# Kernel optimization log

Measured on AMD Instinct MI355X. Metric: run time of the kernel, lower is better.

The kernel has to match this reference:

```python
import jax, jax.numpy as jnp
import numpy as np

B, T, D, F, E, TOPK = 4, 2048, 1024, 2752, 8, 2


def setup_inputs() -> dict:
    key = jax.random.key(0)
    k1, k2, k3, k4 = jax.random.split(key, 4)
    x = jax.random.normal(k1, (B, T, D), dtype=jnp.float32)
    # Expert params, torch Linear(bias=False) stored as [in, out] for x @ W
    W13 = jax.random.normal(k2, (E, D, 2 * F), dtype=jnp.float32) * 0.02  # gate+up packed
    W2 = jax.random.normal(k3, (E, F, D), dtype=jnp.float32) * 0.02       # down proj
    Wr = jax.random.normal(k4, (D, E), dtype=jnp.float32) * 0.02          # router
    return {"x": x, "W13": W13, "W2": W2, "Wr": Wr}


def reference(x, W13, W2, Wr):
    b, t, d = x.shape
    xf = x.reshape(-1, d)                       # [N, D]
    n = xf.shape[0]
    logits = xf @ Wr                            # [N, E]
    probs = jax.nn.softmax(logits, axis=-1)
    top_probs, top_idx = jax.lax.top_k(probs, TOPK)  # [N, K]
    top_probs = top_probs / top_probs.sum(axis=-1, keepdims=True)
    # combine weights: cw[n, e] = sum_k top_probs[n, k] * (top_idx[n, k] == e)
    cw = jnp.zeros((n, E), dtype=xf.dtype).at[jnp.arange(n)[:, None], top_idx].add(top_probs)
    out = jnp.zeros_like(xf)
    for e in range(E):  # small fixed expert loop; tokens with cw==0 contribute nothing
        x13 = xf @ W13[e]                       # [N, 2F]
        x1, x3 = jnp.split(x13, 2, axis=-1)
        h = jax.nn.silu(x1) * x3                # SwiGLU
        out = out + cw[:, e:e + 1] * (h @ W2[e])
    return out.reshape(b, t, d)
```

## Files before the change

kernel.cpp:

```cpp
#include <hip/hip_runtime.h>
#include <stdint.h>

#define NTOK 8192
#define DDIM 1024
#define FDIM 2752
#define NEXP 8
#define DF2  5504
#define NSLOT 16384
#define NT1 16
#define NT2 43

typedef __attribute__((ext_vector_type(8))) short bf16x8;
typedef __attribute__((ext_vector_type(4))) float f32x4;
typedef __attribute__((ext_vector_type(4))) unsigned short u16x4;
typedef __attribute__((ext_vector_type(8))) unsigned short u16x8;

constexpr size_t XB_OFF   = 0;
constexpr size_t XB_SZ    = (size_t)NTOK * DDIM * 2;
constexpr size_t W13T_OFF = XB_OFF + XB_SZ;
constexpr size_t W13T_SZ  = (size_t)NEXP * DF2 * DDIM * 2;
constexpr size_t W2T_OFF  = W13T_OFF + W13T_SZ;
constexpr size_t W2T_SZ   = (size_t)NEXP * DDIM * FDIM * 2;
constexpr size_t H_OFF    = W2T_OFF + W2T_SZ;
constexpr size_t H_SZ     = (size_t)NSLOT * FDIM * 2;
constexpr size_t ST_OFF   = H_OFF + H_SZ;
constexpr size_t SW_OFF   = ST_OFF + (size_t)NSLOT * 4;
constexpr size_t TTI_OFF  = SW_OFF + (size_t)NSLOT * 4;
constexpr size_t TTW_OFF  = TTI_OFF + (size_t)NTOK * 8;
constexpr size_t META_OFF = TTW_OFF + (size_t)NTOK * 8;
constexpr size_t TS_OFF   = META_OFF + 256;

__device__ __forceinline__ unsigned short f2bf(float f) {
  unsigned u = __float_as_uint(f);
  u += 0x7FFFu + ((u >> 16) & 1u);
  return (unsigned short)(u >> 16);
}

__device__ __forceinline__ void gl_lds16(const void* g, void* l) {
  __builtin_amdgcn_global_load_lds(
      (const __attribute__((address_space(1))) unsigned int*)g,
      (__attribute__((address_space(3))) unsigned int*)l, 16, 0, 0);
}

#define BARF()  do { asm volatile("" ::: "memory"); __builtin_amdgcn_s_barrier(); asm volatile("" ::: "memory"); } while (0)
#define LGKM0   asm volatile("s_waitcnt lgkmcnt(0)" ::: "memory")
#define GATE6   asm volatile("s_waitcnt vmcnt(6)" ::: "memory")
#define GATE4   asm volatile("s_waitcnt vmcnt(4)" ::: "memory")
#define VM0     asm volatile("s_waitcnt vmcnt(0)" ::: "memory")
#define PRIO1   __builtin_amdgcn_s_setprio(1)
#define PRIO0   __builtin_amdgcn_s_setprio(0)
#define MFMA16(aa, bb, cc) cc = __builtin_amdgcn_mfma_f32_16x16x32_bf16(aa, bb, cc, 0, 0, 0)

#define STG(dstbase, parr, koff)                        \
  do {                                                  \
    gl_lds16(parr[0] + (koff), (dstbase) + sdst);       \
    gl_lds16(parr[1] + (koff), (dstbase) + sdst + 512); \
  } while (0)

__global__ void cvt_x_k(const float* __restrict__ x, unsigned short* __restrict__ xb) {
  int i = blockIdx.x * 256 + threadIdx.x;
  float4 v = ((const float4*)x)[i];
  u16x4 o;
  o[0] = f2bf(v.x); o[1] = f2bf(v.y); o[2] = f2bf(v.z); o[3] = f2bf(v.w);
  ((u16x4*)xb)[i] = o;
}

__global__ void tcvt_k(const float* __restrict__ src, unsigned short* __restrict__ dst,
                       int R, int C) {
  __shared__ unsigned short tile[64][65];
  long base = (long)blockIdx.z * R * C;
  src += base; dst += base;
  int r0 = blockIdx.y * 64, c0 = blockIdx.x * 64;
  int t = threadIdx.x;
  int rr = t >> 4, cc = (t & 15) * 4;
  for (int i = 0; i < 4; ++i) {
    float4 v = *(const float4*)&src[(long)(r0 + rr + i * 16) * C + c0 + cc];
    tile[rr + i * 16][cc + 0] = f2bf(v.x);
    tile[rr + i * 16][cc + 1] = f2bf(v.y);
    tile[rr + i * 16][cc + 2] = f2bf(v.z);
    tile[rr + i * 16][cc + 3] = f2bf(v.w);
  }
  __syncthreads();
  int dr = t >> 2, sg = (t & 3) * 16;
  u16x8 o0, o1;
  for (int i = 0; i < 8; ++i) { o0[i] = tile[sg + i][dr]; o1[i] = tile[sg + 8 + i][dr]; }
  unsigned short* dp = &dst[(long)(c0 + dr) * R + r0 + sg];
  *(u16x8*)dp = o0;
  *(u16x8*)(dp + 8) = o1;
}

__global__ void router_k(const float* __restrict__ x, const float* __restrict__ Wr,
                         int* __restrict__ meta, int2* __restrict__ tt_i,
                         float2* __restrict__ tt_w) {
  int lane = threadIdx.x & 63;
  int tok = blockIdx.x * 4 + (threadIdx.x >> 6);
  float acc[8];
#pragma unroll
  for (int e = 0; e < 8; ++e) acc[e] = 0.f;
  const float4* xr = (const float4*)(x + (long)tok * DDIM);
#pragma unroll
  for (int it = 0; it < 4; ++it) {
    float4 v = xr[it * 64 + lane];
    int d = (it * 64 + lane) * 4;
    float xv[4] = {v.x, v.y, v.z, v.w};
#pragma unroll
    for (int j = 0; j < 4; ++j) {
      const float4* wr = (const float4*)(Wr + (long)(d + j) * NEXP);
      float4 wa = wr[0], wb = wr[1];
      acc[0] += xv[j] * wa.x; acc[1] += xv[j] * wa.y;
      acc[2] += xv[j] * wa.z; acc[3] += xv[j] * wa.w;
      acc[4] += xv[j] * wb.x; acc[5] += xv[j] * wb.y;
      acc[6] += xv[j] * wb.z; acc[7] += xv[j] * wb.w;
    }
  }
#pragma unroll
  for (int e = 0; e < 8; ++e)
    for (int off = 32; off; off >>= 1) acc[e] += __shfl_xor(acc[e], off, 64);
  if (lane == 0) {
    float m = acc[0];
    for (int e = 1; e < 8; ++e) m = fmaxf(m, acc[e]);
    float p[8];
    for (int e = 0; e < 8; ++e) p[e] = __expf(acc[e] - m);
    int e0 = 0;
    for (int e = 1; e < 8; ++e) if (p[e] > p[e0]) e0 = e;
    int e1 = -1;
    for (int e = 0; e < 8; ++e) { if (e == e0) continue; if (e1 < 0 || p[e] > p[e1]) e1 = e; }
    float s = p[e0] + p[e1];
    atomicAdd(&meta[e0], 1);
    atomicAdd(&meta[e1], 1);
    tt_i[tok] = make_int2(e0, e1);
    tt_w[tok] = make_float2(p[e0] / s, p[e1] / s);
  }
}

__global__ void offsets_k(int* meta) {
  int run = 0;
  for (int e = 0; e < NEXP; ++e) { meta[16 + e] = run; run += meta[e]; }
}

__global__ void scatter_k(const int2* __restrict__ tt_i, const float2* __restrict__ tt_w,
                          int* __restrict__ meta, int* __restrict__ slot_tok,
                          float* __restrict__ slot_w, int2* __restrict__ tok_slot) {
  int n = blockIdx.x * 256 + threadIdx.x;
  int2 ei = tt_i[n];
  float2 wv = tt_w[n];
  int p0 = atomicAdd(&meta[8 + ei.x], 1);
  int s0 = meta[16 + ei.x] + p0;
  slot_tok[s0] = n; slot_w[s0] = wv.x;
  int p1 = atomicAdd(&meta[8 + ei.y], 1);
  int s1 = meta[16 + ei.y] + p1;
  slot_tok[s1] = n; slot_w[s1] = wv.y;
  tok_slot[n] = make_int2(s0, s1);
}

__global__ __launch_bounds__(512, 2) void gemm1_k(
    const unsigned short* __restrict__ xb, const unsigned short* __restrict__ w13t,
    const int* __restrict__ meta, const int* __restrict__ slot_tok,
    unsigned short* __restrict__ h) {
  int e = blockIdx.z;
  int n_e = meta[e];
  int m0 = blockIdx.y * 256;
  if (m0 >= n_e) return;
  int base = meta[16 + e];
  int c0 = blockIdx.x * 128;
  const unsigned short* wB = w13t + (long)e * DF2 * DDIM;

  __shared__ unsigned short Ab[2][2][8192];
  __shared__ unsigned short Bb[2][2][8192];

  int t = threadIdx.x;
  int lane = t & 63, w = t >> 6;
  int wm = w >> 2, wn = w & 3;
  int fr = lane & 15;

  int rj = w * 16 + (lane >> 3);
  int kc = ((lane & 7) ^ ((lane >> 4) & 2)) * 8;
  int sdst = w * 1024 + lane * 8;

  const unsigned short* pA[2][2];
  const unsigned short* pB[2][2];
#pragma unroll
  for (int hh = 0; hh < 2; ++hh)
#pragma unroll
    for (int j = 0; j < 2; ++j) {
      int tr = hh * 128 + rj + j * 8;
      int tok = slot_tok[base + min(m0 + tr, n_e - 1)];
      pA[hh][j] = xb + (long)tok * DDIM + kc;
      int wr = (tr < 128) ? min(c0 + tr, FDIM - 1) : FDIM + min(c0 + tr - 128, FDIM - 1);
      pB[hh][j] = wB + (long)wr * DDIM + kc;
    }

  int qp = ((lane >> 4) ^ ((lane >> 2) & 1) * 2) * 8;
  int abase = fr * 64 + qp;
  int bbase = wn * 2048 + fr * 64 + qp;

  f32x4 acc[8][4];
#pragma unroll
  for (int mi = 0; mi < 8; ++mi)
#pragma unroll
    for (int n = 0; n < 4; ++n) acc[mi][n] = (f32x4){0.f, 0.f, 0.f, 0.f};
  bf16x8 a[8], b0, b1;

  STG(&Ab[0][0][0], pA[0], 0);
  STG(&Ab[0][1][0], pA[1], 0);
  STG(&Bb[0][0][0], pB[0], 0);
  STG(&Bb[0][1][0], pB[1], 0);
  STG(&Bb[1][0][0], pB[0], (1 < NT1) ? 64 : 0);
  GATE4;
  BARF();

#pragma unroll 1
  for (int U = 0; U < NT1; ++U) {
    int cur = U & 1, nxt = cur ^ 1;
    const unsigned short* Ac = &Ab[cur][wm][0];
    const unsigned short* B0c = &Bb[cur][0][0];
    const unsigned short* B1c = &Bb[cur][1][0];
    int k1 = ((U + 1) < NT1) ? (U + 1) * 64 : 0;
    int k2 = ((U + 2) < NT1) ? (U + 2) * 64 : 0;
#pragma unroll
    for (int mi = 0; mi < 8; ++mi) a[mi] = *(const bf16x8*)&Ac[mi * 1024 + abase];
    b0 = *(const bf16x8*)&B0c[bbase];
    b1 = *(const bf16x8*)&B0c[1024 + bbase];
    STG(&Ab[nxt][0][0], pA[0], k1);
    BARF(); LGKM0;
    PRIO1;
#pragma unroll
    for (int mi = 0; mi < 8; ++mi) { MFMA16(a[mi], b0, acc[mi][0]); MFMA16(a[mi], b1, acc[mi][1]); }
    PRIO0;
    GATE4;
    BARF();
    b0 = *(const bf16x8*)&B1c[bbase];
    b1 = *(const bf16x8*)&B1c[1024 + bbase];
    STG(&Ab[nxt][1][0], pA[1], k1);
    BARF(); LGKM0;
    PRIO1;
#pragma unroll
    for (int mi = 0; mi < 8; ++mi) { MFMA16(a[mi], b0, acc[mi][2]); MFMA16(a[mi], b1, acc[mi][3]); }
    PRIO0;
    BARF();
#pragma unroll
    for (int mi = 0; mi < 8; ++mi) a[mi] = *(const bf16x8*)&Ac[mi * 1024 + 32 + abase];
    b0 = *(const bf16x8*)&B0c[32 + bbase];
    b1 = *(const bf16x8*)&B0c[1024 + 32 + bbase];
    STG(&Bb[nxt][1][0], pB[1], k1);
    BARF(); LGKM0;
    PRIO1;
#pragma unroll
    for (int mi = 0; mi < 8; ++mi) { MFMA16(a[mi], b0, acc[mi][0]); MFMA16(a[mi], b1, acc[mi][1]); }
    PRIO0;
    GATE6;
    BARF();
    b0 = *(const bf16x8*)&B1c[32 + bbase];
    b1 = *(const bf16x8*)&B1c[1024 + 32 + bbase];
    STG(&Bb[cur][0][0], pB[0], k2);
    BARF(); LGKM0;
    PRIO1;
#pragma unroll
    for (int mi = 0; mi < 8; ++mi) { MFMA16(a[mi], b0, acc[mi][2]); MFMA16(a[mi], b1, acc[mi][3]); }
    PRIO0;
    GATE4;
    BARF();
  }
  VM0;

  int quad = lane >> 4;
#pragma unroll
  for (int mi = 0; mi < 8; ++mi)
#pragma unroll
    for (int r = 0; r < 4; ++r) {
      int m = m0 + wm * 128 + mi * 16 + quad * 4 + r;
      if (m < n_e) {
        unsigned short* hp = &h[(long)(base + m) * FDIM];
#pragma unroll
        for (int n = 0; n < 2; ++n) {
          int col = c0 + wn * 32 + n * 16 + fr;
          if (col < FDIM) {
            float g = acc[mi][n][r], u = acc[mi][n + 2][r];
            hp[col] = f2bf((g / (1.f + __expf(-g))) * u);
          }
        }
      }
    }
}

__global__ __launch_bounds__(512, 2) void gemm2_k(
    const unsigned short* __restrict__ hb, const unsigned short* __restrict__ w2t,
    const int* __restrict__ meta, const float* __restrict__ slot_w,
    float* __restrict__ y) {
  int e = blockIdx.z;
  int n_e = meta[e];
  int m0 = blockIdx.y * 256;
  if (m0 >= n_e) return;
  int base = meta[16 + e];
  int c0 = blockIdx.x * 256;
  const unsigned short* wB = w2t + (long)e * DDIM * FDIM;

  __shared__ unsigned short Ab[2][2][8192];
  __shared__ unsigned short Bb[2][2][8192];

  int t = threadIdx.x;
  int lane = t & 63, w = t >> 6;
  int wm = w >> 2, wn = w & 3;
  int fr = lane & 15;

  int rj = w * 16 + (lane >> 3);
  int kc = ((lane & 7) ^ ((lane >> 4) & 2)) * 8;
  int sdst = w * 1024 + lane * 8;

  const unsigned short* pA[2][2];
  const unsigned short* pB[2][2];
#pragma unroll
  for (int hh = 0; hh < 2; ++hh)
#pragma unroll
    for (int j = 0; j < 2; ++j) {
      int tr = hh * 128 + rj + j * 8;
      int srow = base + min(m0 + tr, n_e - 1);
      pA[hh][j] = hb + (long)srow * FDIM + kc;
      pB[hh][j] = wB + (long)(c0 + tr) * FDIM + kc;
    }

  int qp = ((lane >> 4) ^ ((lane >> 2) & 1) * 2) * 8;
  int abase = fr * 64 + qp;
  int bbase = wn * 2048 + fr * 64 + qp;

  f32x4 acc[8][4];
#pragma unroll
  for (int mi = 0; mi < 8; ++mi)
#pragma unroll
    for (int n = 0; n < 4; ++n) acc[mi][n] = (f32x4){0.f, 0.f, 0.f, 0.f};
  bf16x8 a[8], b0, b1;

  STG(&Ab[0][0][0], pA[0], 0);
  STG(&Ab[0][1][0], pA[1], 0);
  STG(&Bb[0][0][0], pB[0], 0);
  STG(&Bb[0][1][0], pB[1], 0);
  STG(&Bb[1][0][0], pB[0], (1 < NT2) ? 64 : 0);
  GATE4;
  BARF();

#pragma unroll 1
  for (int U = 0; U < NT2; ++U) {
    int cur = U & 1, nxt = cur ^ 1;
    const unsigned short* Ac = &Ab[cur][wm][0];
    const unsigned short* B0c = &Bb[cur][0][0];
    const unsigned short* B1c = &Bb[cur][1][0];
    int k1 = ((U + 1) < NT2) ? (U + 1) * 64 : 0;
    int k2 = ((U + 2) < NT2) ? (U + 2) * 64 : 0;
#pragma unroll
    for (int mi = 0; mi < 8; ++mi) a[mi] = *(const bf16x8*)&Ac[mi * 1024 + abase];
    b0 = *(const bf16x8*)&B0c[bbase];
    b1 = *(const bf16x8*)&B0c[1024 + bbase];
    STG(&Ab[nxt][0][0], pA[0], k1);
    BARF(); LGKM0;
    PRIO1;
#pragma unroll
    for (int mi = 0; mi < 8; ++mi) { MFMA16(a[mi], b0, acc[mi][0]); MFMA16(a[mi], b1, acc[mi][1]); }
    PRIO0;
    GATE4;
    BARF();
    b0 = *(const bf16x8*)&B1c[bbase];
    b1 = *(const bf16x8*)&B1c[1024 + bbase];
    STG(&Ab[nxt][1][0], pA[1], k1);
    BARF(); LGKM0;
    PRIO1;
#pragma unroll
    for (int mi = 0; mi < 8; ++mi) { MFMA16(a[mi], b0, acc[mi][2]); MFMA16(a[mi], b1, acc[mi][3]); }
    PRIO0;
    BARF();
#pragma unroll
    for (int mi = 0; mi < 8; ++mi) a[mi] = *(const bf16x8*)&Ac[mi * 1024 + 32 + abase];
    b0 = *(const bf16x8*)&B0c[32 + bbase];
    b1 = *(const bf16x8*)&B0c[1024 + 32 + bbase];
    STG(&Bb[nxt][1][0], pB[1], k1);
    BARF(); LGKM0;
    PRIO1;
#pragma unroll
    for (int mi = 0; mi < 8; ++mi) { MFMA16(a[mi], b0, acc[mi][0]); MFMA16(a[mi], b1, acc[mi][1]); }
    PRIO0;
    GATE6;
    BARF();
    b0 = *(const bf16x8*)&B1c[32 + bbase];
    b1 = *(const bf16x8*)&B1c[1024 + 32 + bbase];
    STG(&Bb[cur][0][0], pB[0], k2);
    BARF(); LGKM0;
    PRIO1;
#pragma unroll
    for (int mi = 0; mi < 8; ++mi) { MFMA16(a[mi], b0, acc[mi][2]); MFMA16(a[mi], b1, acc[mi][3]); }
    PRIO0;
    GATE4;
    BARF();
  }
  VM0;

  int quad = lane >> 4;
#pragma unroll
  for (int mi = 0; mi < 8; ++mi)
#pragma unroll
    for (int r = 0; r < 4; ++r) {
      int m = m0 + wm * 128 + mi * 16 + quad * 4 + r;
      if (m < n_e) {
        float wgt = slot_w[base + m];
        float* yp = y + (long)(base + m) * DDIM;
#pragma unroll
        for (int n = 0; n < 4; ++n) {
          int col = c0 + (n >> 1) * 128 + wn * 32 + (n & 1) * 16 + fr;
          yp[col] = wgt * acc[mi][n][r];
        }
      }
    }
}

__global__ void combine_k(const float* __restrict__ y, const int2* __restrict__ tok_slot,
                          float* __restrict__ out) {
  int tok = blockIdx.x * 4 + (threadIdx.x >> 6);
  int lane = threadIdx.x & 63;
  int2 s = tok_slot[tok];
  const float4* y0 = (const float4*)(y + (long)s.x * DDIM);
  const float4* y1 = (const float4*)(y + (long)s.y * DDIM);
  float4* o = (float4*)(out + (long)tok * DDIM);
#pragma unroll
  for (int i = 0; i < 4; ++i) {
    float4 u = y0[i * 64 + lane], v = y1[i * 64 + lane];
    o[i * 64 + lane] = make_float4(u.x + v.x, u.y + v.y, u.z + v.z, u.w + v.w);
  }
}

extern "C" void kernel_launch(void* const* d_in, const int* in_sizes, int n_in,
                              void* d_out, int out_size, void* d_ws, size_t ws_size,
                              hipStream_t stream) {
  const float* x   = (const float*)d_in[0];
  const float* W13 = (const float*)d_in[1];
  const float* W2  = (const float*)d_in[2];
  const float* Wr  = (const float*)d_in[3];
  float* out = (float*)d_out;
  char* ws = (char*)d_ws;

  unsigned short* xb   = (unsigned short*)(ws + XB_OFF);
  unsigned short* w13t = (unsigned short*)(ws + W13T_OFF);
  unsigned short* w2t  = (unsigned short*)(ws + W2T_OFF);
  unsigned short* hbuf = (unsigned short*)(ws + H_OFF);
  int*    slot_tok = (int*)(ws + ST_OFF);
  float*  slot_w   = (float*)(ws + SW_OFF);
  int2*   tt_i     = (int2*)(ws + TTI_OFF);
  float2* tt_w     = (float2*)(ws + TTW_OFF);
  int*    meta     = (int*)(ws + META_OFF);
  int2*   tok_slot = (int2*)(ws + TS_OFF);
  float*  ybuf     = (float*)(ws + W13T_OFF);

  hipMemsetAsync(meta, 0, 128, stream);

  cvt_x_k<<<NTOK * DDIM / 4 / 256, 256, 0, stream>>>(x, xb);
  tcvt_k<<<dim3(DF2 / 64, DDIM / 64, NEXP), 256, 0, stream>>>(W13, w13t, DDIM, DF2);
  tcvt_k<<<dim3(DDIM / 64, FDIM / 64, NEXP), 256, 0, stream>>>(W2, w2t, FDIM, DDIM);
  router_k<<<NTOK / 4, 256, 0, stream>>>(x, Wr, meta, tt_i, tt_w);
  offsets_k<<<1, 1, 0, stream>>>(meta);
  scatter_k<<<NTOK / 256, 256, 0, stream>>>(tt_i, tt_w, meta, slot_tok, slot_w, tok_slot);
  gemm1_k<<<dim3(FDIM / 128 + 1, NTOK / 256, NEXP), 512, 0, stream>>>(xb, w13t, meta, slot_tok, hbuf);
  gemm2_k<<<dim3(DDIM / 256, NTOK / 256, NEXP), 512, 0, stream>>>(hbuf, w2t, meta, slot_w, ybuf);
  combine_k<<<NTOK / 4, 256, 0, stream>>>(ybuf, tok_slot, out);
}
```

Before: 1.113 ms.

## Split LDS tiles into two K-halves with 32-wide rows and simpler prefetch

Both grouped GEMM kernels change their LDS staging layout. Each 64-wide K tile is now stored as two 32-element K-half planes (offset 4096) with a new XOR swizzle, instead of 64-element rows. Each thread now issues one row pointer per half-tile, with the second load offset by 32 in K, which cuts per-thread address registers. The B-tile early prefetch (k2 into the current buffer) is dropped in favour of a plain double buffer with a vmcnt(2) gate. This simplifies the schedule and may change bank-conflict behaviour, but it reduces how far global loads run ahead of compute.

```diff
diff --git a/kernel.cpp b/kernel.cpp
--- a/kernel.cpp
+++ b/kernel.cpp
@@ -44,17 +44,16 @@
 
 #define BARF()  do { asm volatile("" ::: "memory"); __builtin_amdgcn_s_barrier(); asm volatile("" ::: "memory"); } while (0)
 #define LGKM0   asm volatile("s_waitcnt lgkmcnt(0)" ::: "memory")
-#define GATE6   asm volatile("s_waitcnt vmcnt(6)" ::: "memory")
-#define GATE4   asm volatile("s_waitcnt vmcnt(4)" ::: "memory")
+#define GATE2   asm volatile("s_waitcnt vmcnt(2)" ::: "memory")
 #define VM0     asm volatile("s_waitcnt vmcnt(0)" ::: "memory")
 #define PRIO1   __builtin_amdgcn_s_setprio(1)
 #define PRIO0   __builtin_amdgcn_s_setprio(0)
 #define MFMA16(aa, bb, cc) cc = __builtin_amdgcn_mfma_f32_16x16x32_bf16(aa, bb, cc, 0, 0, 0)
 
-#define STG(dstbase, parr, koff)                        \
-  do {                                                  \
-    gl_lds16(parr[0] + (koff), (dstbase) + sdst);       \
-    gl_lds16(parr[1] + (koff), (dstbase) + sdst + 512); \
+#define STG(dstbase, p, koff)                               \
+  do {                                                      \
+    gl_lds16((p) + (koff), (dstbase) + sdst);               \
+    gl_lds16((p) + (koff) + 32, (dstbase) + sdst + 4096);   \
   } while (0)
 
 __global__ void cvt_x_k(const float* __restrict__ x, unsigned short* __restrict__ xb) {
@@ -173,26 +172,24 @@
   int wm = w >> 2, wn = w & 3;
   int fr = lane & 15;
 
-  int rj = w * 16 + (lane >> 3);
-  int kc = ((lane & 7) ^ ((lane >> 4) & 2)) * 8;
-  int sdst = w * 1024 + lane * 8;
-
-  const unsigned short* pA[2][2];
-  const unsigned short* pB[2][2];
-#pragma unroll
-  for (int hh = 0; hh < 2; ++hh)
-#pragma unroll
-    for (int j = 0; j < 2; ++j) {
-      int tr = hh * 128 + rj + j * 8;
-      int tok = slot_tok[base + min(m0 + tr, n_e - 1)];
-      pA[hh][j] = xb + (long)tok * DDIM + kc;
-      int wr = (tr < 128) ? min(c0 + tr, FDIM - 1) : FDIM + min(c0 + tr - 128, FDIM - 1);
-      pB[hh][j] = wB + (long)wr * DDIM + kc;
-    }
-
-  int qp = ((lane >> 4) ^ ((lane >> 2) & 1) * 2) * 8;
-  int abase = fr * 64 + qp;
-  int bbase = wn * 2048 + fr * 64 + qp;
+  int rj = lane >> 2;
+  int kc = ((lane & 3) ^ ((lane >> 5) & 1) * 2) * 8;
+  int sdst = w * 512 + lane * 8;
+
+  const unsigned short* pA[2];
+  const unsigned short* pB[2];
+#pragma unroll
+  for (int hh = 0; hh < 2; ++hh) {
+    int tr = hh * 128 + w * 16 + rj;
+    int tok = slot_tok[base + min(m0 + tr, n_e - 1)];
+    pA[hh] = xb + (long)tok * DDIM + kc;
+    int wr = hh * FDIM + min(c0 + w * 16 + rj, FDIM - 1);
+    pB[hh] = wB + (long)wr * DDIM + kc;
+  }
+
+  int qp = ((lane >> 4) ^ ((fr >> 3) & 1) * 2) * 8;
+  int abase = fr * 32 + qp;
+  int bbase = wn * 1024 + fr * 32 + qp;
 
   f32x4 acc[8][4];
 #pragma unroll
@@ -205,8 +202,7 @@
   STG(&Ab[0][1][0], pA[1], 0);
   STG(&Bb[0][0][0], pB[0], 0);
   STG(&Bb[0][1][0], pB[1], 0);
-  STG(&Bb[1][0][0], pB[0], (1 < NT1) ? 64 : 0);
-  GATE4;
+  VM0;
   BARF();
 
 #pragma unroll 1
@@ -216,21 +212,20 @@
     const unsigned short* B0c = &Bb[cur][0][0];
     const unsigned short* B1c = &Bb[cur][1][0];
     int k1 = ((U + 1) < NT1) ? (U + 1) * 64 : 0;
-    int k2 = ((U + 2) < NT1) ? (U + 2) * 64 : 0;
-#pragma unroll
-    for (int mi = 0; mi < 8; ++mi) a[mi] = *(const bf16x8*)&Ac[mi * 1024 + abase];
+#pragma unroll
+    for (int mi = 0; mi < 8; ++mi) a[mi] = *(const bf16x8*)&Ac[mi * 512 + abase];
     b0 = *(const bf16x8*)&B0c[bbase];
-    b1 = *(const bf16x8*)&B0c[1024 + bbase];
+    b1 = *(const bf16x8*)&B0c[512 + bbase];
     STG(&Ab[nxt][0][0], pA[0], k1);
     BARF(); LGKM0;
     PRIO1;
 #pragma unroll
     for (int mi = 0; mi < 8; ++mi) { MFMA16(a[mi], b0, acc[mi][0]); MFMA16(a[mi], b1, acc[mi][1]); }
     PRIO0;
-    GATE4;
+    GATE2;
     BARF();
     b0 = *(const bf16x8*)&B1c[bbase];
-    b1 = *(const bf16x8*)&B1c[1024 + bbase];
+    b1 = *(const bf16x8*)&B1c[512 + bbase];
     STG(&Ab[nxt][1][0], pA[1], k1);
     BARF(); LGKM0;
     PRIO1;
@@ -239,26 +234,25 @@
     PRIO0;
     BARF();
 #pragma unroll
-    for (int mi = 0; mi < 8; ++mi) a[mi] = *(const bf16x8*)&Ac[mi * 1024 + 32 + abase];
-    b0 = *(const bf16x8*)&B0c[32 + bbase];
-    b1 = *(const bf16x8*)&B0c[1024 + 32 + bbase];
+    for (int mi = 0; mi < 8; ++mi) a[mi] = *(const bf16x8*)&Ac[4096 + mi * 512 + abase];
+    b0 = *(const bf16x8*)&B0c[4096 + bbase];
+    b1 = *(const bf16x8*)&B0c[4096 + 512 + bbase];
+    STG(&Bb[nxt][0][0], pB[0], k1);
+    BARF(); LGKM0;
+    PRIO1;
+#pragma unroll
+    for (int mi = 0; mi < 8; ++mi) { MFMA16(a[mi], b0, acc[mi][0]); MFMA16(a[mi], b1, acc[mi][1]); }
+    PRIO0;
+    BARF();
+    b0 = *(const bf16x8*)&B1c[4096 + bbase];
+    b1 = *(const bf16x8*)&B1c[4096 + 512 + bbase];
     STG(&Bb[nxt][1][0], pB[1], k1);
     BARF(); LGKM0;
     PRIO1;
 #pragma unroll
-    for (int mi = 0; mi < 8; ++mi) { MFMA16(a[mi], b0, acc[mi][0]); MFMA16(a[mi], b1, acc[mi][1]); }
-    PRIO0;
-    GATE6;
-    BARF();
-    b0 = *(const bf16x8*)&B1c[32 + bbase];
-    b1 = *(const bf16x8*)&B1c[1024 + 32 + bbase];
-    STG(&Bb[cur][0][0], pB[0], k2);
-    BARF(); LGKM0;
-    PRIO1;
-#pragma unroll
     for (int mi = 0; mi < 8; ++mi) { MFMA16(a[mi], b0, acc[mi][2]); MFMA16(a[mi], b1, acc[mi][3]); }
     PRIO0;
-    GATE4;
+    GATE2;
     BARF();
   }
   VM0;
@@ -303,25 +297,23 @@
   int wm = w >> 2, wn = w & 3;
   int fr = lane & 15;
 
-  int rj = w * 16 + (lane >> 3);
-  int kc = ((lane & 7) ^ ((lane >> 4) & 2)) * 8;
-  int sdst = w * 1024 + lane * 8;
-
-  const unsigned short* pA[2][2];
-  const unsigned short* pB[2][2];
-#pragma unroll
-  for (int hh = 0; hh < 2; ++hh)
-#pragma unroll
-    for (int j = 0; j < 2; ++j) {
-      int tr = hh * 128 + rj + j * 8;
-      int srow = base + min(m0 + tr, n_e - 1);
-      pA[hh][j] = hb + (long)srow * FDIM + kc;
-      pB[hh][j] = wB + (long)(c0 + tr) * FDIM + kc;
-    }
-
-  int qp = ((lane >> 4) ^ ((lane >> 2) & 1) * 2) * 8;
-  int abase = fr * 64 + qp;
-  int bbase = wn * 2048 + fr * 64 + qp;
+  int rj = lane >> 2;
+  int kc = ((lane & 3) ^ ((lane >> 5) & 1) * 2) * 8;
+  int sdst = w * 512 + lane * 8;
+
+  const unsigned short* pA[2];
+  const unsigned short* pB[2];
+#pragma unroll
+  for (int hh = 0; hh < 2; ++hh) {
+    int tr = hh * 128 + w * 16 + rj;
+    int srow = base + min(m0 + tr, n_e - 1);
+    pA[hh] = hb + (long)srow * FDIM + kc;
+    pB[hh] = wB + (long)(c0 + tr) * FDIM + kc;
+  }
+
+  int qp = ((lane >> 4) ^ ((fr >> 3) & 1) * 2) * 8;
+  int abase = fr * 32 + qp;
+  int bbase = wn * 1024 + fr * 32 + qp;
 
   f32x4 acc[8][4];
 #pragma unroll
@@ -334,8 +326,7 @@
   STG(&Ab[0][1][0], pA[1], 0);
   STG(&Bb[0][0][0], pB[0], 0);
   STG(&Bb[0][1][0], pB[1], 0);
-  STG(&Bb[1][0][0], pB[0], (1 < NT2) ? 64 : 0);
-  GATE4;
+  VM0;
   BARF();
 
 #pragma unroll 1
@@ -345,21 +336,20 @@
     const unsigned short* B0c = &Bb[cur][0][0];
     const unsigned short* B1c = &Bb[cur][1][0];
     int k1 = ((U + 1) < NT2) ? (U + 1) * 64 : 0;
-    int k2 = ((U + 2) < NT2) ? (U + 2) * 64 : 0;
-#pragma unroll
-    for (int mi = 0; mi < 8; ++mi) a[mi] = *(const bf16x8*)&Ac[mi * 1024 + abase];
+#pragma unroll
+    for (int mi = 0; mi < 8; ++mi) a[mi] = *(const bf16x8*)&Ac[mi * 512 + abase];
     b0 = *(const bf16x8*)&B0c[bbase];
-    b1 = *(const bf16x8*)&B0c[1024 + bbase];
+    b1 = *(const bf16x8*)&B0c[512 + bbase];
     STG(&Ab[nxt][0][0], pA[0], k1);
     BARF(); LGKM0;
     PRIO1;
 #pragma unroll
     for (int mi = 0; mi < 8; ++mi) { MFMA16(a[mi], b0, acc[mi][0]); MFMA16(a[mi], b1, acc[mi][1]); }
     PRIO0;
-    GATE4;
+    GATE2;
     BARF();
     b0 = *(const bf16x8*)&B1c[bbase];
-    b1 = *(const bf16x8*)&B1c[1024 + bbase];
+    b1 = *(const bf16x8*)&B1c[512 + bbase];
     STG(&Ab[nxt][1][0], pA[1], k1);
     BARF(); LGKM0;
     PRIO1;
@@ -368,26 +358,25 @@
     PRIO0;
     BARF();
 #pragma unroll
-    for (int mi = 0; mi < 8; ++mi) a[mi] = *(const bf16x8*)&Ac[mi * 1024 + 32 + abase];
-    b0 = *(const bf16x8*)&B0c[32 + bbase];
-    b1 = *(const bf16x8*)&B0c[1024 + 32 + bbase];
+    for (int mi = 0; mi < 8; ++mi) a[mi] = *(const bf16x8*)&Ac[4096 + mi * 512 + abase];
+    b0 = *(const bf16x8*)&B0c[4096 + bbase];
+    b1 = *(const bf16x8*)&B0c[4096 + 512 + bbase];
+    STG(&Bb[nxt][0][0], pB[0], k1);
+    BARF(); LGKM0;
+    PRIO1;
+#pragma unroll
+    for (int mi = 0; mi < 8; ++mi) { MFMA16(a[mi], b0, acc[mi][0]); MFMA16(a[mi], b1, acc[mi][1]); }
+    PRIO0;
+    BARF();
+    b0 = *(const bf16x8*)&B1c[4096 + bbase];
+    b1 = *(const bf16x8*)&B1c[4096 + 512 + bbase];
     STG(&Bb[nxt][1][0], pB[1], k1);
     BARF(); LGKM0;
     PRIO1;
 #pragma unroll
-    for (int mi = 0; mi < 8; ++mi) { MFMA16(a[mi], b0, acc[mi][0]); MFMA16(a[mi], b1, acc[mi][1]); }
-    PRIO0;
-    GATE6;
-    BARF();
-    b0 = *(const bf16x8*)&B1c[32 + bbase];
-    b1 = *(const bf16x8*)&B1c[1024 + 32 + bbase];
-    STG(&Bb[cur][0][0], pB[0], k2);
-    BARF(); LGKM0;
-    PRIO1;
-#pragma unroll
     for (int mi = 0; mi < 8; ++mi) { MFMA16(a[mi], b0, acc[mi][2]); MFMA16(a[mi], b1, acc[mi][3]); }
     PRIO0;
-    GATE4;
+    GATE2;
     BARF();
   }
   VM0;
```

Result: faster. 1.064 ms (-4.4%).
